# Optimization experiments

Hardware: AMD Instinct MI355X
Metric: run time of the kernel (lower is better)

The kernel has to match this reference:

```python
import jax, jax.numpy as jnp
import numpy as np


def reference(x, coef_ref, coef_qry):
    # x: [B, Hr, Wr, Hq, Wq] similarity tensor
    B, Hr, Wr, Hq, Wq = x.shape
    xr = x.reshape(B, Hr * Wr, Hq * Wq)  # [B, R, Q]
    # softmax over ref axis (axis=1) of coef_ref * (x - max over axis 1)
    xm_ref = xr - jnp.max(xr, axis=1, keepdims=True)
    conf_ref = jax.nn.softmax(coef_ref[0] * xm_ref, axis=1)
    # softmax over qry axis (axis=2) of coef_qry * (x - max over axis 2)
    xm_qry = xr - jnp.max(xr, axis=2, keepdims=True)
    conf_qry = jax.nn.softmax(coef_qry[0] * xm_qry, axis=2)
    confidence = jnp.sqrt(conf_ref * conf_qry)  # [B, R, Q]
    # top_k(k=1) over last axis + gather_nd of that value == max over axis 2
    values = jnp.max(confidence, axis=2)  # [B, R]
    return values.reshape(B, Hr, Wr, 1)


def setup_inputs() -> dict:
    key = jax.random.key(0)
    k1, = jax.random.split(key, 1)
    B, Hr, Wr, Hq, Wq = 16, 64, 64, 32, 32
    alpha = 10.0
    x = jax.random.normal(k1, (B, Hr, Wr, Hq, Wq), dtype=jnp.float32)
    coef_ref = jnp.full((1,), alpha, dtype=jnp.float32)
    coef_qry = jnp.full((1,), alpha, dtype=jnp.float32)
    return {"x": x, "coef_ref": coef_ref, "coef_qry": coef_qry}
```

## Files before the change

kernel.cpp:

```cpp
#include <hip/hip_runtime.h>
#include <math.h>
#include <stdint.h>


constexpr int B = 16;
constexpr int R = 4096;
constexpr int Q = 1024;
constexpr int CAP4 = 16;
#define DELTA 0.9f

__device__ __forceinline__ float wmax64(float v) {
#pragma unroll
    for (int o = 32; o; o >>= 1) v = fmaxf(v, __shfl_xor(v, o, 64));
    return v;
}
__device__ __forceinline__ float wsum64(float v) {
#pragma unroll
    for (int o = 32; o; o >>= 1) v += __shfl_xor(v, o, 64);
    return v;
}
__device__ __forceinline__ float max4(float4 v) {
    return fmaxf(fmaxf(v.x, v.y), fmaxf(v.z, v.w));
}
__device__ __forceinline__ float sum4(float4 v) {
    return (v.x + v.y) + (v.z + v.w);
}
__device__ __forceinline__ float4 exp4(float a, float4 v) {
    return make_float4(__expf(a * v.x), __expf(a * v.y),
                       __expf(a * v.z), __expf(a * v.w));
}
__device__ __forceinline__ void add4(float4& d, float4 s) {
    d.x += s.x; d.y += s.y; d.z += s.z; d.w += s.w;
}

__global__ __launch_bounds__(256) void qatm_pass1(
    const float* __restrict__ x,
    float* __restrict__ psum,
    float* __restrict__ rmArr,
    float* __restrict__ rsArr,
    uint32_t* __restrict__ cntArr,
    float4* __restrict__ cand4,
    uint32_t* __restrict__ candg,
    const float* __restrict__ coef_ref,
    const float* __restrict__ coef_qry)
{
    const int blk = blockIdx.x;
    const int b = blk >> 6, chunk = blk & 63;
    const int w = threadIdx.x >> 6, l = threadIdx.x & 63;
    const float ar = coef_ref[0], aq = coef_qry[0];
    const bool same = (ar == aq);
    const uint64_t lanemask = (1ull << l) - 1ull;

    const size_t row0 = (size_t)b * R + (size_t)chunk * 64 + (size_t)w * 16;
    const float4* xb = reinterpret_cast<const float4*>(x) + row0 * (Q / 4);

    float4 cs0{0,0,0,0}, cs1{0,0,0,0}, cs2{0,0,0,0}, cs3{0,0,0,0};

    for (int rr = 0; rr < 16; ++rr) {
        const float4* xr = xb + (size_t)rr * (Q / 4);
        float4 v0 = xr[l], v1 = xr[64 + l], v2 = xr[128 + l], v3 = xr[192 + l];

        float g0 = max4(v0), g1 = max4(v1), g2 = max4(v2), g3 = max4(v3);
        float rm = wmax64(fmaxf(fmaxf(g0, g1), fmaxf(g2, g3)));

        float4 e0 = exp4(ar, v0), e1 = exp4(ar, v1),
               e2 = exp4(ar, v2), e3 = exp4(ar, v3);
        add4(cs0, e0); add4(cs1, e1); add4(cs2, e2); add4(cs3, e3);

        float rsum;
        if (same) {
            rsum = (sum4(e0) + sum4(e1)) + (sum4(e2) + sum4(e3));
        } else {
            rsum = (sum4(exp4(aq, v0)) + sum4(exp4(aq, v1))) +
                   (sum4(exp4(aq, v2)) + sum4(exp4(aq, v3)));
        }
        rsum = wsum64(rsum);

        const float th = rm - DELTA;
        uint32_t cnt = 0;
        const size_t grow = row0 + rr;
        float4* cbase = cand4 + grow * CAP4;
        uint32_t* gbase = candg + grow * CAP4;

#define CAND4(gm, vec, gi)                                                  \
        {                                                                   \
            bool p = (gm) >= th;                                            \
            uint64_t mk = __ballot(p);                                      \
            uint32_t off = cnt + (uint32_t)__popcll(mk & lanemask);         \
            if (p && off < CAP4) { cbase[off] = (vec); gbase[off] = (gi); } \
            cnt += (uint32_t)__popcll(mk);                                  \
        }
        CAND4(g0, v0, (uint32_t)l)
        CAND4(g1, v1, (uint32_t)(64 + l))
        CAND4(g2, v2, (uint32_t)(128 + l))
        CAND4(g3, v3, (uint32_t)(192 + l))
#undef CAND4

        if (l == 0) { rmArr[grow] = rm; rsArr[grow] = rsum; cntArr[grow] = cnt; }
    }

    __shared__ float4 sh[4][256];
    sh[w][l] = cs0; sh[w][64 + l] = cs1; sh[w][128 + l] = cs2; sh[w][192 + l] = cs3;
    __syncthreads();
    const int t = threadIdx.x;
    float4 a = sh[0][t], b4 = sh[1][t], c4 = sh[2][t], d4 = sh[3][t];
    float4 s;
    s.x = (a.x + b4.x) + (c4.x + d4.x);
    s.y = (a.y + b4.y) + (c4.y + d4.y);
    s.z = (a.z + b4.z) + (c4.z + d4.z);
    s.w = (a.w + b4.w) + (c4.w + d4.w);
    reinterpret_cast<float4*>(psum)[(size_t)blk * 256 + t] = s;
}

__global__ __launch_bounds__(256) void qatm_combine(
    const float* __restrict__ psum, float* __restrict__ cvec)
{
    const int tid = blockIdx.x * 256 + threadIdx.x;
    const int b = tid >> 10, q = tid & (Q - 1);
    float s = 0.f;
#pragma unroll 8
    for (int i = 0; i < 64; ++i) s += psum[(size_t)(b * 64 + i) * 1024 + q];
    cvec[tid] = __logf(s);
}

__global__ __launch_bounds__(256) void qatm_cmin(
    const float* __restrict__ cvec, float* __restrict__ cminArr)
{
    const int b = blockIdx.x, t = threadIdx.x;
    float4 c = reinterpret_cast<const float4*>(cvec)[b * 256 + t];
    float m = fminf(fminf(c.x, c.y), fminf(c.z, c.w));
    m = -wmax64(-m);
    __shared__ float sh[4];
    if ((t & 63) == 0) sh[t >> 6] = m;
    __syncthreads();
    if (t == 0) cminArr[b] = fminf(fminf(sh[0], sh[1]), fminf(sh[2], sh[3]));
}

__global__ __launch_bounds__(256) void qatm_select(
    const float* __restrict__ x, const float* __restrict__ cvec,
    const float* __restrict__ cminArr,
    const float* __restrict__ rmArr, const float* __restrict__ rsArr,
    const uint32_t* __restrict__ cntArr,
    const float4* __restrict__ cand4, const uint32_t* __restrict__ candg,
    const float* __restrict__ coef_ref, const float* __restrict__ coef_qry,
    float* __restrict__ out)
{
    const int w = threadIdx.x >> 6, l = threadIdx.x & 63;
    const size_t row = (size_t)blockIdx.x * 4 + w;
    const int b = (int)(row >> 12);
    const float ar = coef_ref[0], aq = coef_qry[0], s2 = ar + aq;

    const uint32_t cnt = cntArr[row];
    const float rm = rmArr[row], rs = rsArr[row];

    float best = -INFINITY;
    bool fallback = (cnt > CAP4);
    if (!fallback) {
        if (l < (int)cnt) {
            float4 v = cand4[row * CAP4 + l];
            uint32_t g = candg[row * CAP4 + l];
            float4 c = reinterpret_cast<const float4*>(cvec)[((size_t)b << 8) + g];
            best = fmaxf(fmaxf(s2 * v.x - c.x, s2 * v.y - c.y),
                         fmaxf(s2 * v.z - c.z, s2 * v.w - c.w));
        }
        best = wmax64(best);
        if (!(best >= s2 * (rm - DELTA) - cminArr[b])) fallback = true;
    }
    if (fallback) {
        const float4* xr = reinterpret_cast<const float4*>(x) + row * (Q / 4);
        const float4* cq = reinterpret_cast<const float4*>(cvec) + ((size_t)b << 8);
        best = -INFINITY;
#pragma unroll
        for (int it = 0; it < 4; ++it) {
            float4 v = xr[it * 64 + l], c = cq[it * 64 + l];
            best = fmaxf(best, fmaxf(fmaxf(s2 * v.x - c.x, s2 * v.y - c.y),
                                     fmaxf(s2 * v.z - c.z, s2 * v.w - c.w)));
        }
        best = wmax64(best);
    }
    if (l == 0) out[row] = __expf(0.5f * (best - __logf(rs)));
}

extern "C" void kernel_launch(void* const* d_in, const int* in_sizes, int n_in,
                              void* d_out, int out_size, void* d_ws, size_t ws_size,
                              hipStream_t stream) {
    const float* x = (const float*)d_in[0];
    const float* coef_ref = (const float*)d_in[1];
    const float* coef_qry = (const float*)d_in[2];
    float* out = (float*)d_out;

    char* ws = (char*)d_ws;
    size_t off = 0;
    float*    psum  = (float*)(ws + off);    off += (size_t)B * 64 * 1024 * 4;
    float4*   cand4 = (float4*)(ws + off);   off += (size_t)B * R * CAP4 * 16;
    uint32_t* candg = (uint32_t*)(ws + off); off += (size_t)B * R * CAP4 * 4;
    float*    cvec  = (float*)(ws + off);    off += (size_t)B * Q * 4;
    float*    rmA   = (float*)(ws + off);    off += (size_t)B * R * 4;
    float*    rsA   = (float*)(ws + off);    off += (size_t)B * R * 4;
    uint32_t* cntA  = (uint32_t*)(ws + off); off += (size_t)B * R * 4;
    float*    cmin  = (float*)(ws + off);

    qatm_pass1<<<B * 64, 256, 0, stream>>>(x, psum, rmA, rsA, cntA, cand4, candg,
                                           coef_ref, coef_qry);
    qatm_combine<<<(B * Q) / 256, 256, 0, stream>>>(psum, cvec);
    qatm_cmin<<<B, 256, 0, stream>>>(cvec, cmin);
    qatm_select<<<(B * R) / 4, 256, 0, stream>>>(x, cvec, cmin, rmA, rsA, cntA,
                                                 cand4, candg, coef_ref, coef_qry, out);
}
```

Measured before the change: 85.67 us.

## Use sampled per-batch threshold for candidates and restructure pass1 to column-per-thread

Adds a sampling kernel that estimates a per-batch candidate threshold from the mean of 32 sampled row maxima, replacing the per-row max threshold. pass1 now gives each thread one float4 column across 64 rows, counts candidates with shared-memory atomics, and reduces row sums through shared memory instead of wave shuffles. The combine and cmin kernels are merged. Correctness still rests on the fallback check, but a threshold from a sample may push many rows into the full-row fallback, or leave some rows with zero candidates, depending on the input distribution.

```diff
diff --git a/kernel.cpp b/kernel.cpp
--- a/kernel.cpp
+++ b/kernel.cpp
@@ -6,128 +6,126 @@
 constexpr int B = 16;
 constexpr int R = 4096;
 constexpr int Q = 1024;
-constexpr int CAP4 = 16;
-#define DELTA 0.9f
+constexpr int CAP = 32;
+#define DTH 0.70f
 
 __device__ __forceinline__ float wmax64(float v) {
 #pragma unroll
     for (int o = 32; o; o >>= 1) v = fmaxf(v, __shfl_xor(v, o, 64));
     return v;
 }
-__device__ __forceinline__ float wsum64(float v) {
-#pragma unroll
-    for (int o = 32; o; o >>= 1) v += __shfl_xor(v, o, 64);
-    return v;
-}
 __device__ __forceinline__ float max4(float4 v) {
     return fmaxf(fmaxf(v.x, v.y), fmaxf(v.z, v.w));
 }
-__device__ __forceinline__ float sum4(float4 v) {
-    return (v.x + v.y) + (v.z + v.w);
-}
-__device__ __forceinline__ float4 exp4(float a, float4 v) {
-    return make_float4(__expf(a * v.x), __expf(a * v.y),
-                       __expf(a * v.z), __expf(a * v.w));
-}
-__device__ __forceinline__ void add4(float4& d, float4 s) {
-    d.x += s.x; d.y += s.y; d.z += s.z; d.w += s.w;
+
+__global__ __launch_bounds__(256) void qatm_sample(const float* __restrict__ x,
+                                                   float* __restrict__ thArr) {
+    const int b = blockIdx.x, t = threadIdx.x;
+    const int k = t >> 3, u = t & 7;
+    const float4* xr = reinterpret_cast<const float4*>(x) +
+                       ((size_t)b * R + (size_t)k * 128) * (Q / 4);
+    float m = -INFINITY;
+#pragma unroll 8
+    for (int i = 0; i < 32; ++i) m = fmaxf(m, max4(xr[u + 8 * i]));
+    m = fmaxf(m, __shfl_xor(m, 1, 64));
+    m = fmaxf(m, __shfl_xor(m, 2, 64));
+    m = fmaxf(m, __shfl_xor(m, 4, 64));
+    __shared__ float sm[32];
+    if (u == 0) sm[k] = m;
+    __syncthreads();
+    if (t == 0) {
+        float s = 0.f;
+#pragma unroll
+        for (int i = 0; i < 32; ++i) s += sm[i];
+        thArr[b] = s * (1.0f / 32.0f) - DTH;
+    }
 }
 
 __global__ __launch_bounds__(256) void qatm_pass1(
     const float* __restrict__ x,
     float* __restrict__ psum,
-    float* __restrict__ rmArr,
     float* __restrict__ rsArr,
     uint32_t* __restrict__ cntArr,
     float4* __restrict__ cand4,
     uint32_t* __restrict__ candg,
+    const float* __restrict__ thArr,
     const float* __restrict__ coef_ref,
     const float* __restrict__ coef_qry)
 {
     const int blk = blockIdx.x;
     const int b = blk >> 6, chunk = blk & 63;
-    const int w = threadIdx.x >> 6, l = threadIdx.x & 63;
+    const int t = threadIdx.x;
     const float ar = coef_ref[0], aq = coef_qry[0];
     const bool same = (ar == aq);
-    const uint64_t lanemask = (1ull << l) - 1ull;
-
-    const size_t row0 = (size_t)b * R + (size_t)chunk * 64 + (size_t)w * 16;
-    const float4* xb = reinterpret_cast<const float4*>(x) + row0 * (Q / 4);
-
-    float4 cs0{0,0,0,0}, cs1{0,0,0,0}, cs2{0,0,0,0}, cs3{0,0,0,0};
-
-    for (int rr = 0; rr < 16; ++rr) {
-        const float4* xr = xb + (size_t)rr * (Q / 4);
-        float4 v0 = xr[l], v1 = xr[64 + l], v2 = xr[128 + l], v3 = xr[192 + l];
-
-        float g0 = max4(v0), g1 = max4(v1), g2 = max4(v2), g3 = max4(v3);
-        float rm = wmax64(fmaxf(fmaxf(g0, g1), fmaxf(g2, g3)));
-
-        float4 e0 = exp4(ar, v0), e1 = exp4(ar, v1),
-               e2 = exp4(ar, v2), e3 = exp4(ar, v3);
-        add4(cs0, e0); add4(cs1, e1); add4(cs2, e2); add4(cs3, e3);
-
-        float rsum;
-        if (same) {
-            rsum = (sum4(e0) + sum4(e1)) + (sum4(e2) + sum4(e3));
-        } else {
-            rsum = (sum4(exp4(aq, v0)) + sum4(exp4(aq, v1))) +
-                   (sum4(exp4(aq, v2)) + sum4(exp4(aq, v3)));
-        }
-        rsum = wsum64(rsum);
-
-        const float th = rm - DELTA;
-        uint32_t cnt = 0;
-        const size_t grow = row0 + rr;
-        float4* cbase = cand4 + grow * CAP4;
-        uint32_t* gbase = candg + grow * CAP4;
-
-#define CAND4(gm, vec, gi)                                                  \
-        {                                                                   \
-            bool p = (gm) >= th;                                            \
-            uint64_t mk = __ballot(p);                                      \
-            uint32_t off = cnt + (uint32_t)__popcll(mk & lanemask);         \
-            if (p && off < CAP4) { cbase[off] = (vec); gbase[off] = (gi); } \
-            cnt += (uint32_t)__popcll(mk);                                  \
-        }
-        CAND4(g0, v0, (uint32_t)l)
-        CAND4(g1, v1, (uint32_t)(64 + l))
-        CAND4(g2, v2, (uint32_t)(128 + l))
-        CAND4(g3, v3, (uint32_t)(192 + l))
-#undef CAND4
-
-        if (l == 0) { rmArr[grow] = rm; rsArr[grow] = rsum; cntArr[grow] = cnt; }
-    }
-
-    __shared__ float4 sh[4][256];
-    sh[w][l] = cs0; sh[w][64 + l] = cs1; sh[w][128 + l] = cs2; sh[w][192 + l] = cs3;
+    const float th = thArr[b];
+    const size_t row0 = (size_t)b * R + (size_t)chunk * 64;
+    const float4* xb = reinterpret_cast<const float4*>(x) + row0 * (Q / 4) + t;
+
+    __shared__ float ssum[16][256];
+    __shared__ int cnt_sh[16];
+    if (t < 16) cnt_sh[t] = 0;
     __syncthreads();
-    const int t = threadIdx.x;
-    float4 a = sh[0][t], b4 = sh[1][t], c4 = sh[2][t], d4 = sh[3][t];
-    float4 s;
-    s.x = (a.x + b4.x) + (c4.x + d4.x);
-    s.y = (a.y + b4.y) + (c4.y + d4.y);
-    s.z = (a.z + b4.z) + (c4.z + d4.z);
-    s.w = (a.w + b4.w) + (c4.w + d4.w);
-    reinterpret_cast<float4*>(psum)[(size_t)blk * 256 + t] = s;
+
+    float4 cs = {0.f, 0.f, 0.f, 0.f};
+
+    for (int win = 0; win < 4; ++win) {
+#pragma unroll 4
+        for (int rr = 0; rr < 16; ++rr) {
+            const int r = win * 16 + rr;
+            float4 v = xb[(size_t)r * 256];
+            float4 e;
+            e.x = __expf(ar * v.x); e.y = __expf(ar * v.y);
+            e.z = __expf(ar * v.z); e.w = __expf(ar * v.w);
+            cs.x += e.x; cs.y += e.y; cs.z += e.z; cs.w += e.w;
+            float rp;
+            if (same) rp = (e.x + e.y) + (e.z + e.w);
+            else rp = (__expf(aq * v.x) + __expf(aq * v.y)) +
+                      (__expf(aq * v.z) + __expf(aq * v.w));
+            ssum[rr][t] = rp;
+            if (max4(v) >= th) {
+                int idx = atomicAdd(&cnt_sh[rr], 1);
+                if (idx < CAP) {
+                    const size_t grow = row0 + r;
+                    cand4[grow * CAP + idx] = v;
+                    candg[grow * CAP + idx] = (uint32_t)t;
+                }
+            }
+        }
+        __syncthreads();
+        const int j = t >> 4, s = t & 15;
+        float p = 0.f;
+#pragma unroll
+        for (int i = 0; i < 16; ++i) p += ssum[j][i * 16 + s];
+        p += __shfl_xor(p, 1, 64);
+        p += __shfl_xor(p, 2, 64);
+        p += __shfl_xor(p, 4, 64);
+        p += __shfl_xor(p, 8, 64);
+        if (s == 0) {
+            const size_t grow = row0 + win * 16 + j;
+            rsArr[grow] = p;
+            cntArr[grow] = (uint32_t)cnt_sh[j];
+            cnt_sh[j] = 0;
+        }
+        __syncthreads();
+    }
+    reinterpret_cast<float4*>(psum)[(size_t)blk * 256 + t] = cs;
 }
 
 __global__ __launch_bounds__(256) void qatm_combine(
-    const float* __restrict__ psum, float* __restrict__ cvec)
-{
-    const int tid = blockIdx.x * 256 + threadIdx.x;
-    const int b = tid >> 10, q = tid & (Q - 1);
-    float s = 0.f;
-#pragma unroll 8
-    for (int i = 0; i < 64; ++i) s += psum[(size_t)(b * 64 + i) * 1024 + q];
-    cvec[tid] = __logf(s);
-}
-
-__global__ __launch_bounds__(256) void qatm_cmin(
-    const float* __restrict__ cvec, float* __restrict__ cminArr)
+    const float* __restrict__ psum, float* __restrict__ cvec,
+    float* __restrict__ cminArr)
 {
     const int b = blockIdx.x, t = threadIdx.x;
-    float4 c = reinterpret_cast<const float4*>(cvec)[b * 256 + t];
+    float4 s = {0.f, 0.f, 0.f, 0.f};
+    const float4* p = reinterpret_cast<const float4*>(psum) + (size_t)b * 64 * 256 + t;
+#pragma unroll 8
+    for (int i = 0; i < 64; ++i) {
+        float4 v = p[(size_t)i * 256];
+        s.x += v.x; s.y += v.y; s.z += v.z; s.w += v.w;
+    }
+    float4 c;
+    c.x = __logf(s.x); c.y = __logf(s.y); c.z = __logf(s.z); c.w = __logf(s.w);
+    reinterpret_cast<float4*>(cvec)[b * 256 + t] = c;
     float m = fminf(fminf(c.x, c.y), fminf(c.z, c.w));
     m = -wmax64(-m);
     __shared__ float sh[4];
@@ -138,9 +136,8 @@
 
 __global__ __launch_bounds__(256) void qatm_select(
     const float* __restrict__ x, const float* __restrict__ cvec,
-    const float* __restrict__ cminArr,
-    const float* __restrict__ rmArr, const float* __restrict__ rsArr,
-    const uint32_t* __restrict__ cntArr,
+    const float* __restrict__ cminArr, const float* __restrict__ thArr,
+    const float* __restrict__ rsArr, const uint32_t* __restrict__ cntArr,
     const float4* __restrict__ cand4, const uint32_t* __restrict__ candg,
     const float* __restrict__ coef_ref, const float* __restrict__ coef_qry,
     float* __restrict__ out)
@@ -149,24 +146,23 @@
     const size_t row = (size_t)blockIdx.x * 4 + w;
     const int b = (int)(row >> 12);
     const float ar = coef_ref[0], aq = coef_qry[0], s2 = ar + aq;
-
     const uint32_t cnt = cntArr[row];
-    const float rm = rmArr[row], rs = rsArr[row];
+    const float rs = rsArr[row];
 
     float best = -INFINITY;
-    bool fallback = (cnt > CAP4);
-    if (!fallback) {
+    bool fb = (cnt > CAP) || (cnt == 0) || !(s2 > 0.f);
+    if (!fb) {
         if (l < (int)cnt) {
-            float4 v = cand4[row * CAP4 + l];
-            uint32_t g = candg[row * CAP4 + l];
+            float4 v = cand4[row * CAP + l];
+            uint32_t g = candg[row * CAP + l];
             float4 c = reinterpret_cast<const float4*>(cvec)[((size_t)b << 8) + g];
             best = fmaxf(fmaxf(s2 * v.x - c.x, s2 * v.y - c.y),
                          fmaxf(s2 * v.z - c.z, s2 * v.w - c.w));
         }
         best = wmax64(best);
-        if (!(best >= s2 * (rm - DELTA) - cminArr[b])) fallback = true;
-    }
-    if (fallback) {
+        if (!(best >= s2 * thArr[b] - cminArr[b])) fb = true;
+    }
+    if (fb) {
         const float4* xr = reinterpret_cast<const float4*>(x) + row * (Q / 4);
         const float4* cq = reinterpret_cast<const float4*>(cvec) + ((size_t)b << 8);
         best = -INFINITY;
@@ -191,19 +187,19 @@
 
     char* ws = (char*)d_ws;
     size_t off = 0;
+    float4*   cand4 = (float4*)(ws + off);   off += (size_t)B * R * CAP * 16;
     float*    psum  = (float*)(ws + off);    off += (size_t)B * 64 * 1024 * 4;
-    float4*   cand4 = (float4*)(ws + off);   off += (size_t)B * R * CAP4 * 16;
-    uint32_t* candg = (uint32_t*)(ws + off); off += (size_t)B * R * CAP4 * 4;
+    uint32_t* candg = (uint32_t*)(ws + off); off += (size_t)B * R * CAP * 4;
     float*    cvec  = (float*)(ws + off);    off += (size_t)B * Q * 4;
-    float*    rmA   = (float*)(ws + off);    off += (size_t)B * R * 4;
     float*    rsA   = (float*)(ws + off);    off += (size_t)B * R * 4;
     uint32_t* cntA  = (uint32_t*)(ws + off); off += (size_t)B * R * 4;
-    float*    cmin  = (float*)(ws + off);
-
-    qatm_pass1<<<B * 64, 256, 0, stream>>>(x, psum, rmA, rsA, cntA, cand4, candg,
-                                           coef_ref, coef_qry);
-    qatm_combine<<<(B * Q) / 256, 256, 0, stream>>>(psum, cvec);
-    qatm_cmin<<<B, 256, 0, stream>>>(cvec, cmin);
-    qatm_select<<<(B * R) / 4, 256, 0, stream>>>(x, cvec, cmin, rmA, rsA, cntA,
+    float*    thA   = (float*)(ws + off);    off += 64;
+    float*    cmin  = (float*)(ws + off);    off += 64;
+
+    qatm_sample<<<B, 256, 0, stream>>>(x, thA);
+    qatm_pass1<<<B * 64, 256, 0, stream>>>(x, psum, rsA, cntA, cand4, candg,
+                                           thA, coef_ref, coef_qry);
+    qatm_combine<<<B, 256, 0, stream>>>(psum, cvec, cmin);
+    qatm_select<<<(B * R) / 4, 256, 0, stream>>>(x, cvec, cmin, thA, rsA, cntA,
                                                  cand4, candg, coef_ref, coef_qry, out);
 }
```

New measurement: 100.1 us. 1.17x slower.
